# Kernel optimization log

Measured on AMD Instinct MI355X. Metric: run time of the kernel, lower is better.

Reference implementation:

```python
import jax, jax.numpy as jnp
import numpy as np

B, N, OBS, ACT, H = 262144, 3, 30, 5, 64
IN = OBS + ACT  # 35
NEG_SLOPE_ATT = 0.2   # PyG GATConv default
NEG_SLOPE_MLP = 0.01
LN_EPS = 1e-5


def setup_inputs() -> dict:
    key = jax.random.key(0)
    ks = jax.random.split(key, 24)
    p = lambda k, shape, s=0.1: jax.random.normal(k, shape, jnp.float32) * s
    return {
        "obs": jax.random.normal(ks[0], (B, N * OBS), jnp.float32),
        "action": jax.random.normal(ks[1], (B, N * ACT), jnp.float32),
        "adj_matrix": jax.random.randint(ks[2], (B, N, N), 0, 2, jnp.int32),
        # GAT layer 1 (in=35 -> out=64, 1 head)
        "W1": p(ks[3], (IN, H)), "a1s": p(ks[4], (H,)), "a1d": p(ks[5], (H,)), "b1": jnp.zeros((H,), jnp.float32),
        # GAT layer 2 (in=64 -> out=64, 1 head)
        "W2": p(ks[6], (H, H)), "a2s": p(ks[7], (H,)), "a2d": p(ks[8], (H,)), "b2": jnp.zeros((H,), jnp.float32),
        # output_net: Linear(192,256)+LN, Linear(256,128)+LN, Linear(128,1)
        "Wo1": p(ks[9], (N * H, 256)), "bo1": jnp.zeros((256,), jnp.float32),
        "g1": jnp.ones((256,), jnp.float32), "be1": jnp.zeros((256,), jnp.float32),
        "Wo2": p(ks[10], (256, 128)), "bo2": jnp.zeros((128,), jnp.float32),
        "g2": jnp.ones((128,), jnp.float32), "be2": jnp.zeros((128,), jnp.float32),
        "Wo3": p(ks[11], (128, 1)), "bo3": jnp.zeros((1,), jnp.float32),
    }


def _gat(x, W, a_s, a_d, b, count):
    # x: [B,N,Din], count[b,i,j] = multiplicity of edge j->i (adj^T + self loop)
    z = jnp.einsum('bnd,de->bne', x, W)                      # [B,N,H]
    s_src = jnp.einsum('bnd,d->bn', z, a_s)                  # score contrib of source j
    s_dst = jnp.einsum('bnd,d->bn', z, a_d)                  # score contrib of target i
    e = jax.nn.leaky_relu(s_src[:, None, :] + s_dst[:, :, None], NEG_SLOPE_ATT)  # e[b,i,j]
    cnt = count.astype(z.dtype)
    m = jnp.max(jnp.where(count > 0, e, -jnp.inf), axis=-1, keepdims=True)  # self-loop guarantees finite
    p = cnt * jnp.exp(e - m)                                 # multiplicity-weighted softmax numerator
    alpha = p / jnp.sum(p, axis=-1, keepdims=True)           # [B,N,N]
    return jnp.einsum('bij,bjd->bid', alpha, z) + b


def _ln(x, g, be):
    mu = jnp.mean(x, axis=-1, keepdims=True)
    v = jnp.mean(jnp.square(x - mu), axis=-1, keepdims=True)
    return (x - mu) * jax.lax.rsqrt(v + LN_EPS) * g + be


def reference(obs, action, adj_matrix, W1, a1s, a1d, b1, W2, a2s, a2d, b2,
              Wo1, bo1, g1, be1, Wo2, bo2, g2, be2, Wo3, bo3):
    Bsz = obs.shape[0]
    x = jnp.concatenate([obs.reshape(Bsz, N, OBS), action.reshape(Bsz, N, ACT)], axis=-1)  # [B,N,35]
    # edge multiplicity: adj[b,s,t] means edge s->t; plus one self-loop per node
    count = jnp.swapaxes(adj_matrix, 1, 2) + jnp.eye(N, dtype=adj_matrix.dtype)  # count[b,i,j]
    h = jax.nn.elu(_gat(x, W1, a1s, a1d, b1, count))
    h = _gat(h, W2, a2s, a2d, b2, count)
    h = h.reshape(Bsz, N * H)
    h = jax.nn.leaky_relu(_ln(h @ Wo1 + bo1, g1, be1), NEG_SLOPE_MLP)
    h = jax.nn.leaky_relu(_ln(h @ Wo2 + bo2, g2, be2), NEG_SLOPE_MLP)
    return h @ Wo3 + bo3  # [B,1]
```

## Files before the change

kernel.cpp:

```cpp
#include <hip/hip_runtime.h>
#include <hip/hip_bf16.h>
#include <stdint.h>

#define B_TOT 262144

typedef __attribute__((ext_vector_type(8))) short bf8;
typedef __attribute__((ext_vector_type(16))) float f32x16;

__device__ __forceinline__ float bf2f(uint32_t u)   { return __uint_as_float(u << 16); }
__device__ __forceinline__ float bfhi2f(uint32_t u) { return __uint_as_float(u & 0xffff0000u); }
__device__ __forceinline__ uint32_t f2bf(float x) {
  uint32_t u = __float_as_uint(x);
  return (u + 0x7fffu + ((u >> 16) & 1u)) >> 16;
}
__device__ __forceinline__ uint32_t pkbf(float lo, float hi) {
  union { __hip_bfloat162 b; uint32_t u; } c;
  c.b = __float22bfloat162_rn(make_float2(lo, hi));
  return c.u;
}
__device__ __forceinline__ bf8 mkfrag(uint32_t w0, uint32_t w1, uint32_t w2, uint32_t w3) {
  union { uint32_t u[4]; bf8 v; } c;
  c.u[0] = w0; c.u[1] = w1; c.u[2] = w2; c.u[3] = w3;
  return c.v;
}

__global__ __launch_bounds__(256) void prep_kernel(
    const int* __restrict__ adj,
    const float* __restrict__ W1, const float* __restrict__ a1s, const float* __restrict__ a1d,
    const float* __restrict__ W2, const float* __restrict__ a2s, const float* __restrict__ a2d,
    const float* __restrict__ Wo1, const float* __restrict__ Wo2,
    uint32_t* __restrict__ cntp, uint16_t* __restrict__ W1F, uint16_t* __restrict__ W2F,
    uint16_t* __restrict__ Wo1F, uint16_t* __restrict__ Wo2F, float* __restrict__ wvec)
{
  const int gid = blockIdx.x * 256 + threadIdx.x;
  if (gid < B_TOT) {
    uint32_t cpv = 0;
    const int* ap = adj + (size_t)gid * 9;
    #pragma unroll
    for (int i = 0; i < 3; ++i)
      #pragma unroll
      for (int j = 0; j < 3; ++j) {
        uint32_t c = (uint32_t)ap[j * 3 + i] + (i == j ? 1u : 0u);
        cpv |= c << (2 * (3 * i + j));
      }
    cntp[gid] = cpv;
  }
  const int e = gid & 7, li = (gid >> 3) & 63;
  const int kfrag = 8 * (e >> 2) + 4 * (li >> 5) + (e & 3);
  if (gid < 3072) {
    const int f = gid >> 9, t = f & 1, ks = f >> 1;
    const int k = ks * 16 + kfrag, row = t * 32 + (li & 31);
    W1F[gid] = (uint16_t)f2bf(k < 35 ? W1[k * 64 + row] : 0.f);
  }
  if (gid < 4096) {
    const int f = gid >> 9, t = f & 1, ks = f >> 1;
    const int k = ks * 16 + kfrag, row = t * 32 + (li & 31);
    W2F[gid] = (uint16_t)f2bf(W2[k * 64 + row]);
  }
  if (gid < 49152) {
    const int rr = gid >> 9, t = rr & 7, ks = rr >> 3;
    const int k = ks * 16 + kfrag, col = t * 32 + (li & 31);
    Wo1F[gid] = (uint16_t)f2bf(Wo1[k * 256 + col]);
  }
  if (gid < 32768) {
    const int rr = gid >> 9, t = rr & 3, ks = rr >> 2;
    const int k = ks * 16 + kfrag, col = t * 32 + (li & 31);
    Wo2F[gid] = (uint16_t)f2bf(Wo2[k * 128 + col]);
  }
  if (gid < 224) {
    if (gid < 48) {
      float s = 0.f; if (gid < 35) for (int d = 0; d < 64; ++d) s += W1[gid * 64 + d] * a1s[d];
      wvec[gid] = s;
    } else if (gid < 96) {
      const int k = gid - 48; float s = 0.f;
      if (k < 35) for (int d = 0; d < 64; ++d) s += W1[k * 64 + d] * a1d[d];
      wvec[64 + k] = s;
    } else if (gid < 160) {
      const int k = gid - 96; float s = 0.f;
      for (int d = 0; d < 64; ++d) s += W2[k * 64 + d] * a2s[d];
      wvec[128 + k] = s;
    } else {
      const int k = gid - 160; float s = 0.f;
      for (int d = 0; d < 64; ++d) s += W2[k * 64 + d] * a2d[d];
      wvec[192 + k] = s;
    }
  }
}

__device__ __forceinline__ void att_alpha(const float (&ss)[3], const float (&sd)[3],
                                          uint32_t cp, float (&al)[3][3])
{
  #pragma unroll
  for (int i = 0; i < 3; ++i) {
    float ev[3]; float mx = -1e30f;
    #pragma unroll
    for (int j = 0; j < 3; ++j) {
      float s = ss[j] + sd[i];
      s = fmaxf(s, 0.2f * s);
      ev[j] = s;
      int c = (cp >> (2 * (3 * i + j))) & 3;
      mx = fmaxf(mx, c ? s : -1e30f);
    }
    float sum = 0.f;
    #pragma unroll
    for (int j = 0; j < 3; ++j) {
      int c = (cp >> (2 * (3 * i + j))) & 3;
      float p = (float)c * __expf(ev[j] - mx);
      al[i][j] = p; sum += p;
    }
    float inv = 1.0f / sum;
    #pragma unroll
    for (int j = 0; j < 3; ++j) al[i][j] *= inv;
  }
}

__device__ __forceinline__ void attention1(const f32x16 (&az)[3][2],
    const float (&ss)[3], const float (&sd)[3], uint32_t cp, int hi,
    const float* __restrict__ bvec, const float* __restrict__ nxs, const float* __restrict__ nxd,
    uint32_t (&Ph)[3][16], float (&ss2)[3], float (&sd2)[3])
{
  float al[3][3];
  att_alpha(ss, sd, cp, al);
  #pragma unroll
  for (int t = 0; t < 2; ++t) {
    float bv[16], nsv[16], ndv[16];
    #pragma unroll
    for (int rq = 0; rq < 4; ++rq) {
      float4 b4 = *reinterpret_cast<const float4*>(bvec + t * 32 + rq * 8 + hi * 4);
      float4 s4 = *reinterpret_cast<const float4*>(nxs + t * 32 + rq * 8 + hi * 4);
      float4 d4 = *reinterpret_cast<const float4*>(nxd + t * 32 + rq * 8 + hi * 4);
      bv[4 * rq + 0] = b4.x; bv[4 * rq + 1] = b4.y; bv[4 * rq + 2] = b4.z; bv[4 * rq + 3] = b4.w;
      nsv[4 * rq + 0] = s4.x; nsv[4 * rq + 1] = s4.y; nsv[4 * rq + 2] = s4.z; nsv[4 * rq + 3] = s4.w;
      ndv[4 * rq + 0] = d4.x; ndv[4 * rq + 1] = d4.y; ndv[4 * rq + 2] = d4.z; ndv[4 * rq + 3] = d4.w;
    }
    #pragma unroll
    for (int i = 0; i < 3; ++i) {
      float hv[16];
      #pragma unroll
      for (int r = 0; r < 16; ++r) {
        float v = bv[r];
        v = fmaf(al[i][0], az[0][t][r], v);
        v = fmaf(al[i][1], az[1][t][r], v);
        v = fmaf(al[i][2], az[2][t][r], v);
        v = v > 0.f ? v : (__expf(v) - 1.f);
        ss2[i] = fmaf(v, nsv[r], ss2[i]); sd2[i] = fmaf(v, ndv[r], sd2[i]);
        hv[r] = v;
      }
      #pragma unroll
      for (int p = 0; p < 8; ++p) Ph[i][t * 8 + p] = pkbf(hv[2 * p], hv[2 * p + 1]);
    }
  }
}

__device__ __forceinline__ void attention2(const f32x16 (&az)[3][2],
    const float (&ss)[3], const float (&sd)[3], uint32_t cp, int hi,
    const float* __restrict__ bvec, uint32_t* __restrict__ ldscol)
{
  float al[3][3];
  att_alpha(ss, sd, cp, al);
  #pragma unroll
  for (int t = 0; t < 2; ++t) {
    float bv[16];
    #pragma unroll
    for (int rq = 0; rq < 4; ++rq) {
      float4 b4 = *reinterpret_cast<const float4*>(bvec + t * 32 + rq * 8 + hi * 4);
      bv[4 * rq + 0] = b4.x; bv[4 * rq + 1] = b4.y; bv[4 * rq + 2] = b4.z; bv[4 * rq + 3] = b4.w;
    }
    #pragma unroll
    for (int i = 0; i < 3; ++i) {
      float hv[16];
      #pragma unroll
      for (int r = 0; r < 16; ++r) {
        float v = bv[r];
        v = fmaf(al[i][0], az[0][t][r], v);
        v = fmaf(al[i][1], az[1][t][r], v);
        v = fmaf(al[i][2], az[2][t][r], v);
        hv[r] = v;
      }
      #pragma unroll
      for (int p = 0; p < 8; ++p)
        ldscol[(i * 16 + t * 8 + p) * 256] = pkbf(hv[2 * p], hv[2 * p + 1]);
    }
  }
}

__global__ __launch_bounds__(256, 2) void fused_kernel(
    const float* __restrict__ obs, const float* __restrict__ act,
    const uint32_t* __restrict__ cntp,
    const uint16_t* __restrict__ W1F, const uint16_t* __restrict__ W2F,
    const float* __restrict__ b1, const float* __restrict__ b2,
    const uint16_t* __restrict__ Wo1F, const float* __restrict__ bo1,
    const float* __restrict__ g1, const float* __restrict__ be1,
    const uint16_t* __restrict__ Wo2F, const float* __restrict__ bo2,
    const float* __restrict__ g2, const float* __restrict__ be2,
    const float* __restrict__ Wo3, const float* __restrict__ bo3,
    const float* __restrict__ wvec, float* __restrict__ out)
{
  __shared__ uint32_t buf[16384];
  const int tid = threadIdx.x;
  const int l = tid & 63, hi = l >> 5, col = l & 31;
  const int w = tid >> 6;
  const int eb = w * 32 + col;
  const int e = blockIdx.x * 128 + eb;
  const uint32_t cp = cntp[e];
  const float* obs_e = obs + (size_t)e * 90;
  const float* act_e = act + (size_t)e * 15;

  f32x16 az[3][2];
  #pragma unroll
  for (int n = 0; n < 3; ++n)
    #pragma unroll
    for (int t = 0; t < 2; ++t)
      #pragma unroll
      for (int r = 0; r < 16; ++r) az[n][t][r] = 0.f;
  float ss1[3] = {0, 0, 0}, sd1[3] = {0, 0, 0};

  #pragma unroll
  for (int ks = 0; ks < 3; ++ks) {
    bf8 xh[3], xl[3];
    #pragma unroll
    for (int n = 0; n < 3; ++n) {
      const float* on = obs_e + n * 30;
      float xv[8];
      #pragma unroll
      for (int r2 = 0; r2 < 2; ++r2) {
        if (ks == 2 && r2 == 1) { xv[4] = xv[5] = xv[6] = xv[7] = 0.f; continue; }
        const int kb = ks * 16 + r2 * 8 + hi * 4;
        #pragma unroll
        for (int j = 0; j < 4; ++j) {
          const int k = kb + j;
          float v = 0.f;
          if (k < 30) v = on[k];
          else if (k < 35) v = act_e[n * 5 + (k - 30)];
          xv[r2 * 4 + j] = v;
        }
        float4 s4 = *reinterpret_cast<const float4*>(wvec + kb);
        float4 d4 = *reinterpret_cast<const float4*>(wvec + 64 + kb);
        ss1[n] = fmaf(xv[r2 * 4 + 0], s4.x, ss1[n]); sd1[n] = fmaf(xv[r2 * 4 + 0], d4.x, sd1[n]);
        ss1[n] = fmaf(xv[r2 * 4 + 1], s4.y, ss1[n]); sd1[n] = fmaf(xv[r2 * 4 + 1], d4.y, sd1[n]);
        ss1[n] = fmaf(xv[r2 * 4 + 2], s4.z, ss1[n]); sd1[n] = fmaf(xv[r2 * 4 + 2], d4.z, sd1[n]);
        ss1[n] = fmaf(xv[r2 * 4 + 3], s4.w, ss1[n]); sd1[n] = fmaf(xv[r2 * 4 + 3], d4.w, sd1[n]);
      }
      uint32_t hw[4], lw[4];
      #pragma unroll
      for (int p = 0; p < 4; ++p) {
        hw[p] = pkbf(xv[2 * p], xv[2 * p + 1]);
        float ra = xv[2 * p]     - bf2f(hw[p]);
        float rb = xv[2 * p + 1] - bfhi2f(hw[p]);
        lw[p] = (__float_as_uint(ra) >> 16) | (__float_as_uint(rb) & 0xffff0000u);
      }
      xh[n] = mkfrag(hw[0], hw[1], hw[2], hw[3]);
      xl[n] = mkfrag(lw[0], lw[1], lw[2], lw[3]);
    }
    #pragma unroll
    for (int t = 0; t < 2; ++t) {
      bf8 a = *reinterpret_cast<const bf8*>(W1F + (size_t)(ks * 2 + t) * 512 + l * 8);
      #pragma unroll
      for (int n = 0; n < 3; ++n) {
        az[n][t] = __builtin_amdgcn_mfma_f32_32x32x16_bf16(a, xh[n], az[n][t], 0, 0, 0);
        az[n][t] = __builtin_amdgcn_mfma_f32_32x32x16_bf16(a, xl[n], az[n][t], 0, 0, 0);
      }
    }
  }
  #pragma unroll
  for (int n = 0; n < 3; ++n) {
    ss1[n] += __shfl_xor(ss1[n], 32);
    sd1[n] += __shfl_xor(sd1[n], 32);
  }

  uint32_t Ph1[3][16];
  float ss2[3] = {0, 0, 0}, sd2[3] = {0, 0, 0};
  attention1(az, ss1, sd1, cp, hi, b1, wvec + 128, wvec + 192, Ph1, ss2, sd2);
  #pragma unroll
  for (int n = 0; n < 3; ++n) {
    ss2[n] += __shfl_xor(ss2[n], 32);
    sd2[n] += __shfl_xor(sd2[n], 32);
  }

  f32x16 a2[3][2];
  #pragma unroll
  for (int n = 0; n < 3; ++n)
    #pragma unroll
    for (int t = 0; t < 2; ++t)
      #pragma unroll
      for (int r = 0; r < 16; ++r) a2[n][t][r] = 0.f;
  #pragma unroll
  for (int ks = 0; ks < 4; ++ks) {
    #pragma unroll
    for (int t = 0; t < 2; ++t) {
      bf8 a = *reinterpret_cast<const bf8*>(W2F + (size_t)(ks * 2 + t) * 512 + l * 8);
      #pragma unroll
      for (int n = 0; n < 3; ++n) {
        bf8 br_ = mkfrag(Ph1[n][4 * ks], Ph1[n][4 * ks + 1], Ph1[n][4 * ks + 2], Ph1[n][4 * ks + 3]);
        a2[n][t] = __builtin_amdgcn_mfma_f32_32x32x16_bf16(a, br_, a2[n][t], 0, 0, 0);
      }
    }
  }

  attention2(a2, ss2, sd2, cp, hi, b2, buf + (hi * 128 + eb));
  __syncthreads();

  const int fb1 = w * 64;
  f32x16 acc[2][4];
  #pragma unroll
  for (int t = 0; t < 2; ++t)
    #pragma unroll
    for (int rq = 0; rq < 4; ++rq) {
      float4 b4 = *reinterpret_cast<const float4*>(bo1 + fb1 + t * 32 + rq * 8 + hi * 4);
      #pragma unroll
      for (int eg = 0; eg < 4; ++eg) {
        acc[t][eg][4 * rq + 0] = b4.x; acc[t][eg][4 * rq + 1] = b4.y;
        acc[t][eg][4 * rq + 2] = b4.z; acc[t][eg][4 * rq + 3] = b4.w;
      }
    }
  #pragma unroll
  for (int ks = 0; ks < 12; ++ks) {
    bf8 bfr[4];
    #pragma unroll
    for (int eg = 0; eg < 4; ++eg) {
      const uint32_t* pc = buf + (hi * 128 + eg * 32 + col) + ks * 4 * 256;
      bfr[eg] = mkfrag(pc[0], pc[256], pc[512], pc[768]);
    }
    #pragma unroll
    for (int t = 0; t < 2; ++t) {
      bf8 a = *reinterpret_cast<const bf8*>(Wo1F + (size_t)(ks * 8 + w * 2 + t) * 512 + l * 8);
      #pragma unroll
      for (int eg = 0; eg < 4; ++eg)
        acc[t][eg] = __builtin_amdgcn_mfma_f32_32x32x16_bf16(a, bfr[eg], acc[t][eg], 0, 0, 0);
    }
  }
  {
    float psm[4], psq[4];
    #pragma unroll
    for (int eg = 0; eg < 4; ++eg) { psm[eg] = 0.f; psq[eg] = 0.f; }
    #pragma unroll
    for (int t = 0; t < 2; ++t)
      #pragma unroll
      for (int eg = 0; eg < 4; ++eg)
        #pragma unroll
        for (int r = 0; r < 16; ++r) {
          const float v = acc[t][eg][r]; psm[eg] += v; psq[eg] = fmaf(v, v, psq[eg]);
        }
    float* part = (float*)buf + 12288;
    #pragma unroll
    for (int eg = 0; eg < 4; ++eg) {
      psm[eg] += __shfl_xor(psm[eg], 32);
      psq[eg] += __shfl_xor(psq[eg], 32);
      if (hi == 0) {
        part[w * 128 + eg * 32 + col] = psm[eg];
        part[512 + w * 128 + eg * 32 + col] = psq[eg];
      }
    }
  }
  __syncthreads();
  float mu1[4], rr1[4];
  {
    const float* part = (const float*)buf + 12288;
    #pragma unroll
    for (int eg = 0; eg < 4; ++eg) {
      const int ei = eg * 32 + col;
      float s = part[ei] + part[128 + ei] + part[256 + ei] + part[384 + ei];
      float q = part[512 + ei] + part[640 + ei] + part[768 + ei] + part[896 + ei];
      mu1[eg] = s * (1.f / 256.f);
      rr1[eg] = rsqrtf(q * (1.f / 256.f) - mu1[eg] * mu1[eg] + 1e-5f);
    }
  }
  __syncthreads();
  #pragma unroll
  for (int t = 0; t < 2; ++t)
    #pragma unroll
    for (int rq = 0; rq < 4; ++rq) {
      float4 gg = *reinterpret_cast<const float4*>(g1 + fb1 + t * 32 + rq * 8 + hi * 4);
      float4 bb = *reinterpret_cast<const float4*>(be1 + fb1 + t * 32 + rq * 8 + hi * 4);
      #pragma unroll
      for (int eg = 0; eg < 4; ++eg) {
        float v0 = (acc[t][eg][4 * rq + 0] - mu1[eg]) * rr1[eg] * gg.x + bb.x; v0 = fmaxf(v0, 0.01f * v0);
        float v1 = (acc[t][eg][4 * rq + 1] - mu1[eg]) * rr1[eg] * gg.y + bb.y; v1 = fmaxf(v1, 0.01f * v1);
        float v2 = (acc[t][eg][4 * rq + 2] - mu1[eg]) * rr1[eg] * gg.z + bb.z; v2 = fmaxf(v2, 0.01f * v2);
        float v3 = (acc[t][eg][4 * rq + 3] - mu1[eg]) * rr1[eg] * gg.w + bb.w; v3 = fmaxf(v3, 0.01f * v3);
        const int c = hi * 128 + eg * 32 + col;
        buf[(w * 16 + t * 8 + rq * 2 + 0) * 256 + c] = pkbf(v0, v1);
        buf[(w * 16 + t * 8 + rq * 2 + 1) * 256 + c] = pkbf(v2, v3);
      }
    }
  __syncthreads();

  const int fb2 = w * 32;
  f32x16 acc2[4];
  #pragma unroll
  for (int rq = 0; rq < 4; ++rq) {
    float4 b4 = *reinterpret_cast<const float4*>(bo2 + fb2 + rq * 8 + hi * 4);
    #pragma unroll
    for (int eg = 0; eg < 4; ++eg) {
      acc2[eg][4 * rq + 0] = b4.x; acc2[eg][4 * rq + 1] = b4.y;
      acc2[eg][4 * rq + 2] = b4.z; acc2[eg][4 * rq + 3] = b4.w;
    }
  }
  #pragma unroll
  for (int ks = 0; ks < 16; ++ks) {
    bf8 bfr[4];
    #pragma unroll
    for (int eg = 0; eg < 4; ++eg) {
      const uint32_t* pc = buf + (hi * 128 + eg * 32 + col) + ks * 4 * 256;
      bfr[eg] = mkfrag(pc[0], pc[256], pc[512], pc[768]);
    }
    bf8 a = *reinterpret_cast<const bf8*>(Wo2F + (size_t)(ks * 4 + w) * 512 + l * 8);
    #pragma unroll
    for (int eg = 0; eg < 4; ++eg)
      acc2[eg] = __builtin_amdgcn_mfma_f32_32x32x16_bf16(a, bfr[eg], acc2[eg], 0, 0, 0);
  }
  __syncthreads();
  {
    float psm[4], psq[4];
    #pragma unroll
    for (int eg = 0; eg < 4; ++eg) { psm[eg] = 0.f; psq[eg] = 0.f; }
    #pragma unroll
    for (int eg = 0; eg < 4; ++eg)
      #pragma unroll
      for (int r = 0; r < 16; ++r) {
        const float v = acc2[eg][r]; psm[eg] += v; psq[eg] = fmaf(v, v, psq[eg]);
      }
    float* part = (float*)buf;
    #pragma unroll
    for (int eg = 0; eg < 4; ++eg) {
      psm[eg] += __shfl_xor(psm[eg], 32);
      psq[eg] += __shfl_xor(psq[eg], 32);
      if (hi == 0) {
        part[w * 128 + eg * 32 + col] = psm[eg];
        part[512 + w * 128 + eg * 32 + col] = psq[eg];
      }
    }
  }
  __syncthreads();
  {
    const float* part = (const float*)buf;
    float* p3 = (float*)buf + 1024;
    float dot[4];
    #pragma unroll
    for (int eg = 0; eg < 4; ++eg) {
      const int ei = eg * 32 + col;
      float s = part[ei] + part[128 + ei] + part[256 + ei] + part[384 + ei];
      float q = part[512 + ei] + part[640 + ei] + part[768 + ei] + part[896 + ei];
      const float mu = s * (1.f / 128.f);
      const float rr = rsqrtf(q * (1.f / 128.f) - mu * mu + 1e-5f);
      float d = 0.f;
      #pragma unroll
      for (int rq = 0; rq < 4; ++rq) {
        float4 gg = *reinterpret_cast<const float4*>(g2 + fb2 + rq * 8 + hi * 4);
        float4 bb = *reinterpret_cast<const float4*>(be2 + fb2 + rq * 8 + hi * 4);
        float4 ww = *reinterpret_cast<const float4*>(Wo3 + fb2 + rq * 8 + hi * 4);
        float v;
        v = (acc2[eg][4 * rq + 0] - mu) * rr * gg.x + bb.x; d = fmaf(fmaxf(v, 0.01f * v), ww.x, d);
        v = (acc2[eg][4 * rq + 1] - mu) * rr * gg.y + bb.y; d = fmaf(fmaxf(v, 0.01f * v), ww.y, d);
        v = (acc2[eg][4 * rq + 2] - mu) * rr * gg.z + bb.z; d = fmaf(fmaxf(v, 0.01f * v), ww.z, d);
        v = (acc2[eg][4 * rq + 3] - mu) * rr * gg.w + bb.w; d = fmaf(fmaxf(v, 0.01f * v), ww.w, d);
      }
      dot[eg] = d;
    }
    #pragma unroll
    for (int eg = 0; eg < 4; ++eg) {
      dot[eg] += __shfl_xor(dot[eg], 32);
      if (hi == 0) p3[w * 128 + eg * 32 + col] = dot[eg];
    }
  }
  __syncthreads();
  if (tid < 128) {
    const float* p3 = (const float*)buf + 1024;
    out[blockIdx.x * 128 + tid] =
        p3[tid] + p3[128 + tid] + p3[256 + tid] + p3[384 + tid] + bo3[0];
  }
}

extern "C" void kernel_launch(void* const* d_in, const int* in_sizes, int n_in,
                              void* d_out, int out_size, void* d_ws, size_t ws_size,
                              hipStream_t stream) {
  const float* obs  = (const float*)d_in[0];
  const float* actn = (const float*)d_in[1];
  const int*   adj  = (const int*)d_in[2];
  const float* W1   = (const float*)d_in[3];
  const float* a1s  = (const float*)d_in[4];
  const float* a1d  = (const float*)d_in[5];
  const float* b1   = (const float*)d_in[6];
  const float* W2   = (const float*)d_in[7];
  const float* a2s  = (const float*)d_in[8];
  const float* a2d  = (const float*)d_in[9];
  const float* b2   = (const float*)d_in[10];
  const float* Wo1  = (const float*)d_in[11];
  const float* bo1  = (const float*)d_in[12];
  const float* g1   = (const float*)d_in[13];
  const float* be1  = (const float*)d_in[14];
  const float* Wo2  = (const float*)d_in[15];
  const float* bo2  = (const float*)d_in[16];
  const float* g2   = (const float*)d_in[17];
  const float* be2  = (const float*)d_in[18];
  const float* Wo3  = (const float*)d_in[19];
  const float* bo3  = (const float*)d_in[20];

  char* ws = (char*)d_ws;
  uint32_t* cntp = (uint32_t*)ws;
  uint16_t* W1F  = (uint16_t*)(ws + 1048576);
  uint16_t* W2F  = (uint16_t*)(ws + 1048576 + 8192);
  uint16_t* Wo1F = (uint16_t*)(ws + 1048576 + 16384);
  uint16_t* Wo2F = (uint16_t*)(ws + 1048576 + 114688);
  float*    wvec = (float*)(ws + 1048576 + 180224);
  float* outp = (float*)d_out;

  prep_kernel<<<1024, 256, 0, stream>>>(adj, W1, a1s, a1d, W2, a2s, a2d, Wo1, Wo2,
                                        cntp, W1F, W2F, Wo1F, Wo2F, wvec);
  fused_kernel<<<2048, 256, 0, stream>>>(obs, actn, cntp, W1F, W2F, b1, b2,
                                         Wo1F, bo1, g1, be1, Wo2F, bo2, g2, be2,
                                         Wo3, bo3, wvec, outp);
}
```

Baseline: 118.1 us.

## Swizzle LDS activation layout for 128-bit reads, drop bf16 split-precision MFMA

Activations staged in shared memory now go into an XOR-swizzled layout of 16-byte rows, so each MFMA B-fragment is one 128-bit LDS load instead of four strided 32-bit loads, and stores become vector writes. The layer-1 input no longer uses a hi/lo bf16 split, which halves the MFMAs in the first GEMM at the cost of lower input precision. The LayerNorm partial sums get their own shared array, which lets two barriers be removed.

```diff
diff --git a/kernel.cpp b/kernel.cpp
--- a/kernel.cpp
+++ b/kernel.cpp
@@ -23,6 +23,10 @@
   c.u[0] = w0; c.u[1] = w1; c.u[2] = w2; c.u[3] = w3;
   return c.v;
 }
+__device__ __forceinline__ bf8 u4bf8(uint4 v) {
+  union { uint4 u; bf8 b; } c; c.u = v; return c.b;
+}
+__device__ __forceinline__ int swz(int c, int q) { return c * 16 + (q ^ (c & 15)); }
 
 __global__ __launch_bounds__(256) void prep_kernel(
     const int* __restrict__ adj,
@@ -154,7 +158,7 @@
 
 __device__ __forceinline__ void attention2(const f32x16 (&az)[3][2],
     const float (&ss)[3], const float (&sd)[3], uint32_t cp, int hi,
-    const float* __restrict__ bvec, uint32_t* __restrict__ ldscol)
+    const float* __restrict__ bvec, uint4* __restrict__ b4p, int c_own)
 {
   float al[3][3];
   att_alpha(ss, sd, cp, al);
@@ -177,9 +181,12 @@
         v = fmaf(al[i][2], az[2][t][r], v);
         hv[r] = v;
       }
-      #pragma unroll
-      for (int p = 0; p < 8; ++p)
-        ldscol[(i * 16 + t * 8 + p) * 256] = pkbf(hv[2 * p], hv[2 * p + 1]);
+      uint32_t w0 = pkbf(hv[0], hv[1]),  w1 = pkbf(hv[2], hv[3]);
+      uint32_t w2 = pkbf(hv[4], hv[5]),  w3 = pkbf(hv[6], hv[7]);
+      uint32_t w4 = pkbf(hv[8], hv[9]),  w5 = pkbf(hv[10], hv[11]);
+      uint32_t w6 = pkbf(hv[12], hv[13]), w7 = pkbf(hv[14], hv[15]);
+      b4p[swz(c_own, i * 4 + t * 2 + 0)] = make_uint4(w0, w1, w2, w3);
+      b4p[swz(c_own, i * 4 + t * 2 + 1)] = make_uint4(w4, w5, w6, w7);
     }
   }
 }
@@ -196,7 +203,10 @@
     const float* __restrict__ Wo3, const float* __restrict__ bo3,
     const float* __restrict__ wvec, float* __restrict__ out)
 {
-  __shared__ uint32_t buf[16384];
+  __shared__ __align__(16) uint32_t buf[16384];
+  __shared__ float part[1536];
+  uint4* b4p = (uint4*)buf;
+  const uint4* b4c = (const uint4*)buf;
   const int tid = threadIdx.x;
   const int l = tid & 63, hi = l >> 5, col = l & 31;
   const int w = tid >> 6;
@@ -217,7 +227,7 @@
 
   #pragma unroll
   for (int ks = 0; ks < 3; ++ks) {
-    bf8 xh[3], xl[3];
+    bf8 xh[3];
     #pragma unroll
     for (int n = 0; n < 3; ++n) {
       const float* on = obs_e + n * 30;
@@ -241,25 +251,15 @@
         ss1[n] = fmaf(xv[r2 * 4 + 2], s4.z, ss1[n]); sd1[n] = fmaf(xv[r2 * 4 + 2], d4.z, sd1[n]);
         ss1[n] = fmaf(xv[r2 * 4 + 3], s4.w, ss1[n]); sd1[n] = fmaf(xv[r2 * 4 + 3], d4.w, sd1[n]);
       }
-      uint32_t hw[4], lw[4];
-      #pragma unroll
-      for (int p = 0; p < 4; ++p) {
-        hw[p] = pkbf(xv[2 * p], xv[2 * p + 1]);
-        float ra = xv[2 * p]     - bf2f(hw[p]);
-        float rb = xv[2 * p + 1] - bfhi2f(hw[p]);
-        lw[p] = (__float_as_uint(ra) >> 16) | (__float_as_uint(rb) & 0xffff0000u);
-      }
-      xh[n] = mkfrag(hw[0], hw[1], hw[2], hw[3]);
-      xl[n] = mkfrag(lw[0], lw[1], lw[2], lw[3]);
+      xh[n] = mkfrag(pkbf(xv[0], xv[1]), pkbf(xv[2], xv[3]),
+                     pkbf(xv[4], xv[5]), pkbf(xv[6], xv[7]));
     }
     #pragma unroll
     for (int t = 0; t < 2; ++t) {
       bf8 a = *reinterpret_cast<const bf8*>(W1F + (size_t)(ks * 2 + t) * 512 + l * 8);
       #pragma unroll
-      for (int n = 0; n < 3; ++n) {
+      for (int n = 0; n < 3; ++n)
         az[n][t] = __builtin_amdgcn_mfma_f32_32x32x16_bf16(a, xh[n], az[n][t], 0, 0, 0);
-        az[n][t] = __builtin_amdgcn_mfma_f32_32x32x16_bf16(a, xl[n], az[n][t], 0, 0, 0);
-      }
     }
   }
   #pragma unroll
@@ -297,7 +297,7 @@
     }
   }
 
-  attention2(a2, ss2, sd2, cp, hi, b2, buf + (hi * 128 + eb));
+  attention2(a2, ss2, sd2, cp, hi, b2, b4p, hi * 128 + eb);
   __syncthreads();
 
   const int fb1 = w * 64;
@@ -317,10 +317,8 @@
   for (int ks = 0; ks < 12; ++ks) {
     bf8 bfr[4];
     #pragma unroll
-    for (int eg = 0; eg < 4; ++eg) {
-      const uint32_t* pc = buf + (hi * 128 + eg * 32 + col) + ks * 4 * 256;
-      bfr[eg] = mkfrag(pc[0], pc[256], pc[512], pc[768]);
-    }
+    for (int eg = 0; eg < 4; ++eg)
+      bfr[eg] = u4bf8(b4c[swz(hi * 128 + eg * 32 + col, ks)]);
     #pragma unroll
     for (int t = 0; t < 2; ++t) {
       bf8 a = *reinterpret_cast<const bf8*>(Wo1F + (size_t)(ks * 8 + w * 2 + t) * 512 + l * 8);
@@ -341,7 +339,6 @@
         for (int r = 0; r < 16; ++r) {
           const float v = acc[t][eg][r]; psm[eg] += v; psq[eg] = fmaf(v, v, psq[eg]);
         }
-    float* part = (float*)buf + 12288;
     #pragma unroll
     for (int eg = 0; eg < 4; ++eg) {
       psm[eg] += __shfl_xor(psm[eg], 32);
@@ -354,35 +351,40 @@
   }
   __syncthreads();
   float mu1[4], rr1[4];
-  {
-    const float* part = (const float*)buf + 12288;
-    #pragma unroll
-    for (int eg = 0; eg < 4; ++eg) {
-      const int ei = eg * 32 + col;
-      float s = part[ei] + part[128 + ei] + part[256 + ei] + part[384 + ei];
-      float q = part[512 + ei] + part[640 + ei] + part[768 + ei] + part[896 + ei];
-      mu1[eg] = s * (1.f / 256.f);
-      rr1[eg] = rsqrtf(q * (1.f / 256.f) - mu1[eg] * mu1[eg] + 1e-5f);
-    }
-  }
-  __syncthreads();
-  #pragma unroll
-  for (int t = 0; t < 2; ++t)
+  #pragma unroll
+  for (int eg = 0; eg < 4; ++eg) {
+    const int ei = eg * 32 + col;
+    float s = part[ei] + part[128 + ei] + part[256 + ei] + part[384 + ei];
+    float q = part[512 + ei] + part[640 + ei] + part[768 + ei] + part[896 + ei];
+    mu1[eg] = s * (1.f / 256.f);
+    rr1[eg] = rsqrtf(q * (1.f / 256.f) - mu1[eg] * mu1[eg] + 1e-5f);
+  }
+  #pragma unroll
+  for (int t = 0; t < 2; ++t) {
+    float gv[16], bv[16];
     #pragma unroll
     for (int rq = 0; rq < 4; ++rq) {
       float4 gg = *reinterpret_cast<const float4*>(g1 + fb1 + t * 32 + rq * 8 + hi * 4);
       float4 bb = *reinterpret_cast<const float4*>(be1 + fb1 + t * 32 + rq * 8 + hi * 4);
-      #pragma unroll
-      for (int eg = 0; eg < 4; ++eg) {
-        float v0 = (acc[t][eg][4 * rq + 0] - mu1[eg]) * rr1[eg] * gg.x + bb.x; v0 = fmaxf(v0, 0.01f * v0);
-        float v1 = (acc[t][eg][4 * rq + 1] - mu1[eg]) * rr1[eg] * gg.y + bb.y; v1 = fmaxf(v1, 0.01f * v1);
-        float v2 = (acc[t][eg][4 * rq + 2] - mu1[eg]) * rr1[eg] * gg.z + bb.z; v2 = fmaxf(v2, 0.01f * v2);
-        float v3 = (acc[t][eg][4 * rq + 3] - mu1[eg]) * rr1[eg] * gg.w + bb.w; v3 = fmaxf(v3, 0.01f * v3);
-        const int c = hi * 128 + eg * 32 + col;
-        buf[(w * 16 + t * 8 + rq * 2 + 0) * 256 + c] = pkbf(v0, v1);
-        buf[(w * 16 + t * 8 + rq * 2 + 1) * 256 + c] = pkbf(v2, v3);
-      }
-    }
+      gv[4 * rq + 0] = gg.x; gv[4 * rq + 1] = gg.y; gv[4 * rq + 2] = gg.z; gv[4 * rq + 3] = gg.w;
+      bv[4 * rq + 0] = bb.x; bv[4 * rq + 1] = bb.y; bv[4 * rq + 2] = bb.z; bv[4 * rq + 3] = bb.w;
+    }
+    #pragma unroll
+    for (int eg = 0; eg < 4; ++eg) {
+      uint32_t wd[8];
+      #pragma unroll
+      for (int p = 0; p < 8; ++p) {
+        float va = (acc[t][eg][2 * p]     - mu1[eg]) * rr1[eg] * gv[2 * p]     + bv[2 * p];
+        float vb = (acc[t][eg][2 * p + 1] - mu1[eg]) * rr1[eg] * gv[2 * p + 1] + bv[2 * p + 1];
+        va = fmaxf(va, 0.01f * va);
+        vb = fmaxf(vb, 0.01f * vb);
+        wd[p] = pkbf(va, vb);
+      }
+      const int c = hi * 128 + eg * 32 + col;
+      b4p[swz(c, w * 4 + t * 2 + 0)] = make_uint4(wd[0], wd[1], wd[2], wd[3]);
+      b4p[swz(c, w * 4 + t * 2 + 1)] = make_uint4(wd[4], wd[5], wd[6], wd[7]);
+    }
+  }
   __syncthreads();
 
   const int fb2 = w * 32;
@@ -400,16 +402,13 @@
   for (int ks = 0; ks < 16; ++ks) {
     bf8 bfr[4];
     #pragma unroll
-    for (int eg = 0; eg < 4; ++eg) {
-      const uint32_t* pc = buf + (hi * 128 + eg * 32 + col) + ks * 4 * 256;
-      bfr[eg] = mkfrag(pc[0], pc[256], pc[512], pc[768]);
-    }
+    for (int eg = 0; eg < 4; ++eg)
+      bfr[eg] = u4bf8(b4c[swz(hi * 128 + eg * 32 + col, ks)]);
     bf8 a = *reinterpret_cast<const bf8*>(Wo2F + (size_t)(ks * 4 + w) * 512 + l * 8);
     #pragma unroll
     for (int eg = 0; eg < 4; ++eg)
       acc2[eg] = __builtin_amdgcn_mfma_f32_32x32x16_bf16(a, bfr[eg], acc2[eg], 0, 0, 0);
   }
-  __syncthreads();
   {
     float psm[4], psq[4];
     #pragma unroll
@@ -420,7 +419,6 @@
       for (int r = 0; r < 16; ++r) {
         const float v = acc2[eg][r]; psm[eg] += v; psq[eg] = fmaf(v, v, psq[eg]);
       }
-    float* part = (float*)buf;
     #pragma unroll
     for (int eg = 0; eg < 4; ++eg) {
       psm[eg] += __shfl_xor(psm[eg], 32);
@@ -433,8 +431,6 @@
   }
   __syncthreads();
   {
-    const float* part = (const float*)buf;
-    float* p3 = (float*)buf + 1024;
     float dot[4];
     #pragma unroll
     for (int eg = 0; eg < 4; ++eg) {
@@ -460,14 +456,13 @@
     #pragma unroll
     for (int eg = 0; eg < 4; ++eg) {
       dot[eg] += __shfl_xor(dot[eg], 32);
-      if (hi == 0) p3[w * 128 + eg * 32 + col] = dot[eg];
+      if (hi == 0) part[1024 + w * 128 + eg * 32 + col] = dot[eg];
     }
   }
   __syncthreads();
   if (tid < 128) {
-    const float* p3 = (const float*)buf + 1024;
-    out[blockIdx.x * 128 + tid] =
-        p3[tid] + p3[128 + tid] + p3[256 + tid] + p3[384 + tid] + bo3[0];
+    out[blockIdx.x * 128 + tid] = part[1024 + tid] + part[1152 + tid] +
+                                  part[1280 + tid] + part[1408 + tid] + bo3[0];
   }
 }
 
```

Measured after the change: 114.0 us. 3.5% less time.
